# Kernel optimization log

Hardware: AMD Instinct MI355X
Metric: run time of the kernel (lower is better)

## Reference

```python
import jax, jax.numpy as jnp
import numpy as np

N_NODES = 10000
N_EDGES = 320000
IN_DIM = 128
HIDDEN = 256
NUM_LAYERS = 6
ALPHA = 0.1
LN_EPS = 1e-5


def setup_inputs() -> dict:
    key = jax.random.key(0)
    ks = jax.random.split(key, 12)
    x = jax.random.normal(ks[0], (N_NODES, IN_DIM), dtype=jnp.float32)
    edge_index = jax.random.randint(ks[1], (2, N_EDGES), 0, N_NODES, dtype=jnp.int64)
    # input MLP params
    W_in = jax.random.normal(ks[2], (IN_DIM, HIDDEN), dtype=jnp.float32) / np.sqrt(IN_DIM)
    b_in = jnp.zeros((HIDDEN,), dtype=jnp.float32)
    g_in = jnp.ones((HIDDEN,), dtype=jnp.float32)
    beta_in = jnp.zeros((HIDDEN,), dtype=jnp.float32)
    # per-layer GCNConv weight/bias + LayerNorm params, stacked over layers
    Wl = jax.random.normal(ks[3], (NUM_LAYERS, HIDDEN, HIDDEN), dtype=jnp.float32) / np.sqrt(HIDDEN)
    bl = jnp.zeros((NUM_LAYERS, HIDDEN), dtype=jnp.float32)
    gl = jnp.ones((NUM_LAYERS, HIDDEN), dtype=jnp.float32)
    betal = jnp.zeros((NUM_LAYERS, HIDDEN), dtype=jnp.float32)
    return {"x": x, "edge_index": edge_index, "W_in": W_in, "b_in": b_in,
            "g_in": g_in, "beta_in": beta_in, "Wl": Wl, "bl": bl,
            "gl": gl, "betal": betal}


def _layernorm(h, g, b):
    mu = jnp.mean(h, axis=-1, keepdims=True)
    var = jnp.var(h, axis=-1, keepdims=True)
    return (h - mu) * jax.lax.rsqrt(var + LN_EPS) * g + b


def reference(x, edge_index, W_in, b_in, g_in, beta_in, Wl, bl, gl, betal):
    N = x.shape[0]
    # input block: Linear -> GELU (exact erf) -> LayerNorm (dropout = eval identity)
    h = jax.nn.gelu(x @ W_in + b_in, approximate=False)
    h = _layernorm(h, g_in, beta_in)

    # GCN normalization with self loops, unit edge weights (edge_weight=None)
    loops = jnp.arange(N, dtype=edge_index.dtype)
    src = jnp.concatenate([edge_index[0], loops])  # [E+N] sources (j)
    dst = jnp.concatenate([edge_index[1], loops])  # [E+N] targets (i)
    w = jnp.ones((src.shape[0],), dtype=x.dtype)
    deg = jax.ops.segment_sum(w, dst, num_segments=N)
    dinv = jnp.where(deg > 0, deg ** -0.5, 0.0)
    norm = dinv[src] * w * dinv[dst]  # [E+N]

    h0 = h
    cur = h
    for l in range(NUM_LAYERS):
        m = cur @ Wl[l]                                        # [N,H] transform
        msgs = norm[:, None] * m[src]                          # gather + scale
        agg = jax.ops.segment_sum(msgs, dst, num_segments=N)   # scatter-add
        agg = agg + bl[l]
        hh = _layernorm(jax.nn.gelu(agg, approximate=False), gl[l], betal[l])
        cur = cur + (1.0 - ALPHA) * hh + ALPHA * h0
    return cur
```

## Files before the change

### kernel.cpp

```cpp
#include <hip/hip_runtime.h>
#include <math.h>

#define N_NODES   10000
#define N_EDGES   320000
#define IN_DIM    128
#define HIDDEN    256
#define NUM_LAYERS 6
#define ALPHA     0.1f
#define LN_EPS    1e-5f

__device__ __forceinline__ float gelu_exact(float x) {
    return 0.5f * x * (1.0f + erff(x * 0.70710678118654752440f));
}

__device__ __forceinline__ float wave_sum64(float v) {
#pragma unroll
    for (int i = 32; i > 0; i >>= 1) v += __shfl_xor(v, i);
    return v;
}


__global__ __launch_bounds__(256) void count_deg_kernel(const int* __restrict__ dst,
                                                        int* __restrict__ cnt) {
    int e = blockIdx.x * 256 + threadIdx.x;
    if (e < N_EDGES) atomicAdd(&cnt[dst[e]], 1);
}

__global__ __launch_bounds__(256) void dinv_kernel(const int* __restrict__ cnt,
                                                   float* __restrict__ dinv) {
    int i = blockIdx.x * 256 + threadIdx.x;
    if (i < N_NODES) dinv[i] = rsqrtf((float)(cnt[i] + 1));
}

__global__ __launch_bounds__(256) void scan_kernel(const int* __restrict__ cnt,
                                                   int* __restrict__ offs) {
    __shared__ int sums[256];
    __shared__ int bases[257];
    int t = threadIdx.x;
    const int chunk = (N_NODES + 255) / 256;
    int b0 = t * chunk;
    int b1 = b0 + chunk; if (b1 > N_NODES) b1 = N_NODES;
    if (b0 > N_NODES) b0 = N_NODES;
    int s = 0;
    for (int i = b0; i < b1; ++i) s += cnt[i];
    sums[t] = s;
    __syncthreads();
    if (t == 0) {
        int r = 0;
        for (int i = 0; i < 256; ++i) { bases[i] = r; r += sums[i]; }
        bases[256] = r;
    }
    __syncthreads();
    int r = bases[t];
    for (int i = b0; i < b1; ++i) { offs[i] = r; r += cnt[i]; }
    if (t == 0) offs[N_NODES] = bases[256];
}

__global__ __launch_bounds__(256) void fill_csr_kernel(const int* __restrict__ src,
                                                       const int* __restrict__ dst,
                                                       const int* __restrict__ offs,
                                                       int* __restrict__ cursor,
                                                       int* __restrict__ csr_src) {
    int e = blockIdx.x * 256 + threadIdx.x;
    if (e < N_EDGES) {
        int d = dst[e], s = src[e];
        int pos = atomicAdd(&cursor[d], 1);
        csr_src[offs[d] + pos] = s;
    }
}

template<int K>
__global__ __launch_bounds__(256) void gemm_kernel(const float* __restrict__ A,
                                                   const float* __restrict__ B,
                                                   float* __restrict__ C) {
    __shared__ float As[16][132];
    __shared__ float Bs[16][68];

    int tid = threadIdx.x;
    int tx = tid & 15;
    int ty = tid >> 4;
    int row0 = blockIdx.x * 128;
    int col0 = blockIdx.y * 64;

    float acc[8][4] = {};

    for (int k0 = 0; k0 < K; k0 += 16) {
        #pragma unroll
        for (int u = 0; u < 2; ++u) {
            int fi = tid * 2 + u;
            int r  = fi >> 2;
            int kk = (fi & 3) * 4;
            int row = row0 + r;
            if (row < N_NODES) {
                const float4 a4 = *(const float4*)&A[(size_t)row * K + k0 + kk];
                As[kk + 0][r] = a4.x; As[kk + 1][r] = a4.y;
                As[kk + 2][r] = a4.z; As[kk + 3][r] = a4.w;
            } else {
                As[kk + 0][r] = 0.f; As[kk + 1][r] = 0.f;
                As[kk + 2][r] = 0.f; As[kk + 3][r] = 0.f;
            }
        }
        {
            int rb = tid >> 4;
            int cb = (tid & 15) * 4;
            const float4 b4 = *(const float4*)&B[(size_t)(k0 + rb) * HIDDEN + col0 + cb];
            *(float4*)&Bs[rb][cb] = b4;
        }
        __syncthreads();

        #pragma unroll
        for (int kk = 0; kk < 16; ++kk) {
            const float4 al = *(const float4*)&As[kk][ty * 8 + 0];
            const float4 ah = *(const float4*)&As[kk][ty * 8 + 4];
            const float4 b4 = *(const float4*)&Bs[kk][tx * 4];
            float a[8] = {al.x, al.y, al.z, al.w, ah.x, ah.y, ah.z, ah.w};
            #pragma unroll
            for (int i = 0; i < 8; ++i) {
                acc[i][0] += a[i] * b4.x;
                acc[i][1] += a[i] * b4.y;
                acc[i][2] += a[i] * b4.z;
                acc[i][3] += a[i] * b4.w;
            }
        }
        __syncthreads();
    }

    #pragma unroll
    for (int i = 0; i < 8; ++i) {
        int row = row0 + ty * 8 + i;
        if (row < N_NODES) {
            float4 v = make_float4(acc[i][0], acc[i][1], acc[i][2], acc[i][3]);
            *(float4*)&C[(size_t)row * HIDDEN + col0 + tx * 4] = v;
        }
    }
}

__global__ __launch_bounds__(256) void ln_in_kernel(const float4* __restrict__ pre,
                                                    const float4* __restrict__ b4,
                                                    const float4* __restrict__ g4,
                                                    const float4* __restrict__ beta4,
                                                    float4* __restrict__ h0,
                                                    float4* __restrict__ cur) {
    int n = blockIdx.x * 4 + (threadIdx.x >> 6);
    int lane = threadIdx.x & 63;
    if (n >= N_NODES) return;

    float4 v = pre[(size_t)n * 64 + lane];
    float4 bb = b4[lane];
    float x0 = gelu_exact(v.x + bb.x);
    float x1 = gelu_exact(v.y + bb.y);
    float x2 = gelu_exact(v.z + bb.z);
    float x3 = gelu_exact(v.w + bb.w);

    float mu = wave_sum64(x0 + x1 + x2 + x3) * (1.0f / 256.0f);
    float d0 = x0 - mu, d1 = x1 - mu, d2 = x2 - mu, d3 = x3 - mu;
    float var = wave_sum64(d0 * d0 + d1 * d1 + d2 * d2 + d3 * d3) * (1.0f / 256.0f);
    float r = rsqrtf(var + LN_EPS);

    float4 gg = g4[lane], be = beta4[lane];
    float4 out = make_float4(d0 * r * gg.x + be.x, d1 * r * gg.y + be.y,
                             d2 * r * gg.z + be.z, d3 * r * gg.w + be.w);
    h0[(size_t)n * 64 + lane]  = out;
    cur[(size_t)n * 64 + lane] = out;
}

__global__ __launch_bounds__(256) void gather_q_kernel(const float4* __restrict__ m4,
                                                       const float* __restrict__ dinv,
                                                       const int* __restrict__ offs,
                                                       const int* __restrict__ csr_src,
                                                       const float4* __restrict__ bias4,
                                                       float4* __restrict__ pre4) {
    int i  = blockIdx.x;
    int q  = (i & 7) >> 1;
    int nb = (i >> 3) * 2 + (i & 1);
    int n  = nb * 4 + (threadIdx.x >> 6);
    int lane = threadIdx.x & 63;
    int g = lane >> 4;
    int t = lane & 15;
    int cbase = q * 16 + t;

    float dn = dinv[n];

    float4 acc = make_float4(0.f, 0.f, 0.f, 0.f);
    if (g == 0) {
        float4 sv = m4[(size_t)n * 64 + cbase];
        float dn2 = dn * dn;
        acc.x = sv.x * dn2; acc.y = sv.y * dn2; acc.z = sv.z * dn2; acc.w = sv.w * dn2;
    }

    int e1 = offs[n + 1];
    int ee = offs[n] + g;
    for (; ee + 12 < e1; ee += 16) {
        int sA = csr_src[ee];
        int sB = csr_src[ee + 4];
        int sC = csr_src[ee + 8];
        int sD = csr_src[ee + 12];
        float4 vA = m4[(size_t)sA * 64 + cbase];
        float4 vB = m4[(size_t)sB * 64 + cbase];
        float4 vC = m4[(size_t)sC * 64 + cbase];
        float4 vD = m4[(size_t)sD * 64 + cbase];
        float wA = dinv[sA] * dn;
        float wB = dinv[sB] * dn;
        float wC = dinv[sC] * dn;
        float wD = dinv[sD] * dn;
        acc.x += wA * vA.x + wB * vB.x + wC * vC.x + wD * vD.x;
        acc.y += wA * vA.y + wB * vB.y + wC * vC.y + wD * vD.y;
        acc.z += wA * vA.z + wB * vB.z + wC * vC.z + wD * vD.z;
        acc.w += wA * vA.w + wB * vB.w + wC * vC.w + wD * vD.w;
    }
    for (; ee < e1; ee += 4) {
        int s = csr_src[ee];
        float4 v = m4[(size_t)s * 64 + cbase];
        float w = dinv[s] * dn;
        acc.x += w * v.x; acc.y += w * v.y; acc.z += w * v.z; acc.w += w * v.w;
    }

    acc.x += __shfl_xor(acc.x, 16);
    acc.y += __shfl_xor(acc.y, 16);
    acc.z += __shfl_xor(acc.z, 16);
    acc.w += __shfl_xor(acc.w, 16);
    acc.x += __shfl_xor(acc.x, 32);
    acc.y += __shfl_xor(acc.y, 32);
    acc.z += __shfl_xor(acc.z, 32);
    acc.w += __shfl_xor(acc.w, 32);

    if (g == 0) {
        float4 bb = bias4[cbase];
        pre4[(size_t)n * 64 + cbase] = make_float4(acc.x + bb.x, acc.y + bb.y,
                                                   acc.z + bb.z, acc.w + bb.w);
    }
}

__global__ __launch_bounds__(256) void ln_res_kernel(const float4* __restrict__ pre4,
                                                     const float4* __restrict__ g4,
                                                     const float4* __restrict__ beta4,
                                                     const float4* __restrict__ h04,
                                                     float4* __restrict__ cur4) {
    int n = blockIdx.x * 4 + (threadIdx.x >> 6);
    int lane = threadIdx.x & 63;
    if (n >= N_NODES) return;

    float4 v = pre4[(size_t)n * 64 + lane];
    float x0 = gelu_exact(v.x);
    float x1 = gelu_exact(v.y);
    float x2 = gelu_exact(v.z);
    float x3 = gelu_exact(v.w);

    float mu = wave_sum64(x0 + x1 + x2 + x3) * (1.0f / 256.0f);
    float d0 = x0 - mu, d1 = x1 - mu, d2 = x2 - mu, d3 = x3 - mu;
    float var = wave_sum64(d0 * d0 + d1 * d1 + d2 * d2 + d3 * d3) * (1.0f / 256.0f);
    float r = rsqrtf(var + LN_EPS);

    float4 gg = g4[lane], be = beta4[lane];
    float h0v = d0 * r * gg.x + be.x;
    float h1v = d1 * r * gg.y + be.y;
    float h2v = d2 * r * gg.z + be.z;
    float h3v = d3 * r * gg.w + be.w;

    size_t idx = (size_t)n * 64 + lane;
    float4 c = cur4[idx];
    float4 h = h04[idx];
    float4 o = make_float4(c.x + (1.0f - ALPHA) * h0v + ALPHA * h.x,
                           c.y + (1.0f - ALPHA) * h1v + ALPHA * h.y,
                           c.z + (1.0f - ALPHA) * h2v + ALPHA * h.z,
                           c.w + (1.0f - ALPHA) * h3v + ALPHA * h.w);
    cur4[idx] = o;
}


extern "C" void kernel_launch(void* const* d_in, const int* in_sizes, int n_in,
                              void* d_out, int out_size, void* d_ws, size_t ws_size,
                              hipStream_t stream) {
    const float* x      = (const float*)d_in[0];
    const int*   ei     = (const int*)  d_in[1];
    const float* W_in   = (const float*)d_in[2];
    const float* b_in   = (const float*)d_in[3];
    const float* g_in   = (const float*)d_in[4];
    const float* bt_in  = (const float*)d_in[5];
    const float* Wl     = (const float*)d_in[6];
    const float* bl     = (const float*)d_in[7];
    const float* gl     = (const float*)d_in[8];
    const float* betal  = (const float*)d_in[9];

    const int* src = ei;
    const int* dst = ei + N_EDGES;

    float* cur = (float*)d_out;

    char* w = (char*)d_ws;
    size_t off = 0;
    auto alloc = [&](size_t bytes) -> void* {
        void* p = w + off;
        off = (off + bytes + 255) & ~(size_t)255;
        return p;
    };
    int*   cnt      = (int*)  alloc(N_NODES * sizeof(int));
    int*   cursor   = (int*)  alloc(N_NODES * sizeof(int));
    int*   offs     = (int*)  alloc((N_NODES + 1) * sizeof(int));
    float* dinv     = (float*)alloc(N_NODES * sizeof(float));
    int*   csr_src  = (int*)  alloc(N_EDGES * sizeof(int));
    float* h0       = (float*)alloc((size_t)N_NODES * HIDDEN * sizeof(float));
    float* m        = (float*)alloc((size_t)N_NODES * HIDDEN * sizeof(float));
    float* pre      = (float*)alloc((size_t)N_NODES * HIDDEN * sizeof(float));

    hipMemsetAsync(cnt,    0, N_NODES * sizeof(int), stream);
    hipMemsetAsync(cursor, 0, N_NODES * sizeof(int), stream);

    const int EB = (N_EDGES + 255) / 256;
    const int NB = (N_NODES + 255) / 256;
    const int NODE_BLOCKS = (N_NODES + 3) / 4;

    count_deg_kernel<<<EB, 256, 0, stream>>>(dst, cnt);
    dinv_kernel<<<NB, 256, 0, stream>>>(cnt, dinv);
    scan_kernel<<<1, 256, 0, stream>>>(cnt, offs);
    fill_csr_kernel<<<EB, 256, 0, stream>>>(src, dst, offs, cursor, csr_src);

    dim3 ggrid((N_NODES + 127) / 128, HIDDEN / 64);

    gemm_kernel<IN_DIM><<<ggrid, 256, 0, stream>>>(x, W_in, m);
    ln_in_kernel<<<NODE_BLOCKS, 256, 0, stream>>>((const float4*)m, (const float4*)b_in,
                                                  (const float4*)g_in, (const float4*)bt_in,
                                                  (float4*)h0, (float4*)cur);

    for (int l = 0; l < NUM_LAYERS; ++l) {
        gemm_kernel<HIDDEN><<<ggrid, 256, 0, stream>>>(cur, Wl + (size_t)l * HIDDEN * HIDDEN, m);
        gather_q_kernel<<<NODE_BLOCKS * 4, 256, 0, stream>>>((const float4*)m, dinv, offs, csr_src,
                                                             (const float4*)(bl + l * HIDDEN),
                                                             (float4*)pre);
        ln_res_kernel<<<NODE_BLOCKS, 256, 0, stream>>>((const float4*)pre,
                                                       (const float4*)(gl + l * HIDDEN),
                                                       (const float4*)(betal + l * HIDDEN),
                                                       (const float4*)h0, (float4*)cur);
    }
}
```

Measured before the change: 552.0 us.

## Replace FP32 SIMT GEMM with split-bf16 MFMA GEMM and pre-transposed weights

The scalar FP32 tiled GEMM is replaced by a matrix-core kernel. Each operand is split into bf16 hi and lo parts, and three MFMA 16x16x32 products (hi*hi, lo*hi, hi*lo) recover close to FP32 accuracy. A prep kernel transposes all layer weights and splits them into hi/lo bf16 arrays once per call, and activations are split on the fly while loading into shared memory. The aim is to cut GEMM compute time, at the cost of some precision loss and an extra prep launch.

```diff
diff --git a/kernel.cpp b/kernel.cpp
--- a/kernel.cpp
+++ b/kernel.cpp
@@ -9,6 +9,9 @@
 #define ALPHA     0.1f
 #define LN_EPS    1e-5f
 
+using bf16x8 = __attribute__((ext_vector_type(8))) __bf16;
+using f32x4  = __attribute__((ext_vector_type(4))) float;
+
 __device__ __forceinline__ float gelu_exact(float x) {
     return 0.5f * x * (1.0f + erff(x * 0.70710678118654752440f));
 }
@@ -17,6 +20,14 @@
 #pragma unroll
     for (int i = 32; i > 0; i >>= 1) v += __shfl_xor(v, i);
     return v;
+}
+
+__device__ __forceinline__ unsigned short f2bf(float f) {
+    unsigned u = __float_as_uint(f);
+    return (unsigned short)((u + 0x7FFF + ((u >> 16) & 1)) >> 16);
+}
+__device__ __forceinline__ float bf2f(unsigned short h) {
+    return __uint_as_float(((unsigned)h) << 16);
 }
 
 
@@ -69,70 +80,124 @@
     }
 }
 
+__global__ __launch_bounds__(256) void prep_w_kernel(const float* __restrict__ Wl,
+                                                     const float* __restrict__ W_in,
+                                                     unsigned short* __restrict__ hi,
+                                                     unsigned short* __restrict__ lo) {
+    int z = blockIdx.z;
+    const float* W;
+    unsigned short *ho, *lg;
+    int K;
+    if (z < 6) {
+        W = Wl + (size_t)z * HIDDEN * HIDDEN; K = HIDDEN;
+        ho = hi + (size_t)z * HIDDEN * HIDDEN;
+        lg = lo + (size_t)z * HIDDEN * HIDDEN;
+    } else {
+        W = W_in; K = IN_DIM;
+        ho = hi + (size_t)6 * HIDDEN * HIDDEN;
+        lg = lo + (size_t)6 * HIDDEN * HIDDEN;
+    }
+    int tk0 = blockIdx.x * 32;
+    if (tk0 >= K) return;
+    int tn0 = blockIdx.y * 32;
+
+    __shared__ float T[32][33];
+    int tx = threadIdx.x & 31, ty = threadIdx.x >> 5;
+    #pragma unroll
+    for (int i = 0; i < 32; i += 8)
+        T[ty + i][tx] = W[(size_t)(tk0 + ty + i) * HIDDEN + tn0 + tx];
+    __syncthreads();
+    #pragma unroll
+    for (int i = 0; i < 32; i += 8) {
+        int n = tn0 + ty + i, k = tk0 + tx;
+        float v = T[tx][ty + i];
+        unsigned short h = f2bf(v);
+        ho[(size_t)n * K + k] = h;
+        lg[(size_t)n * K + k] = f2bf(v - bf2f(h));
+    }
+}
+
 template<int K>
-__global__ __launch_bounds__(256) void gemm_kernel(const float* __restrict__ A,
-                                                   const float* __restrict__ B,
-                                                   float* __restrict__ C) {
-    __shared__ float As[16][132];
-    __shared__ float Bs[16][68];
-
-    int tid = threadIdx.x;
-    int tx = tid & 15;
-    int ty = tid >> 4;
-    int row0 = blockIdx.x * 128;
+__global__ __launch_bounds__(256) void gemm_mfma_kernel(const float* __restrict__ A,
+                                                        const unsigned short* __restrict__ Bh,
+                                                        const unsigned short* __restrict__ Bl,
+                                                        float* __restrict__ C) {
+    __shared__ unsigned short AsH[64][40];
+    __shared__ unsigned short AsL[64][40];
+    __shared__ unsigned short BsH[64][40];
+    __shared__ unsigned short BsL[64][40];
+
+    int tid  = threadIdx.x;
+    int row0 = blockIdx.x * 64;
     int col0 = blockIdx.y * 64;
 
-    float acc[8][4] = {};
-
-    for (int k0 = 0; k0 < K; k0 += 16) {
+    int l  = tid & 63, w = tid >> 6;
+    int wr = w >> 1, wc = w & 1;
+    int r  = l & 15, kb = l >> 4;
+
+    f32x4 acc00 = {0.f, 0.f, 0.f, 0.f};
+    f32x4 acc01 = acc00, acc10 = acc00, acc11 = acc00;
+
+    for (int k0 = 0; k0 < K; k0 += 32) {
+        __syncthreads();
         #pragma unroll
         for (int u = 0; u < 2; ++u) {
             int fi = tid * 2 + u;
-            int r  = fi >> 2;
-            int kk = (fi & 3) * 4;
-            int row = row0 + r;
-            if (row < N_NODES) {
-                const float4 a4 = *(const float4*)&A[(size_t)row * K + k0 + kk];
-                As[kk + 0][r] = a4.x; As[kk + 1][r] = a4.y;
-                As[kk + 2][r] = a4.z; As[kk + 3][r] = a4.w;
-            } else {
-                As[kk + 0][r] = 0.f; As[kk + 1][r] = 0.f;
-                As[kk + 2][r] = 0.f; As[kk + 3][r] = 0.f;
-            }
+            int row = fi >> 3, f4 = fi & 7;
+            float4 a = make_float4(0.f, 0.f, 0.f, 0.f);
+            if (row0 + row < N_NODES)
+                a = *(const float4*)&A[(size_t)(row0 + row) * K + k0 + f4 * 4];
+            unsigned short h0 = f2bf(a.x), h1 = f2bf(a.y), h2 = f2bf(a.z), h3 = f2bf(a.w);
+            *(short4*)&AsH[row][f4 * 4] = make_short4((short)h0, (short)h1, (short)h2, (short)h3);
+            *(short4*)&AsL[row][f4 * 4] = make_short4((short)f2bf(a.x - bf2f(h0)),
+                                                      (short)f2bf(a.y - bf2f(h1)),
+                                                      (short)f2bf(a.z - bf2f(h2)),
+                                                      (short)f2bf(a.w - bf2f(h3)));
         }
-        {
-            int rb = tid >> 4;
-            int cb = (tid & 15) * 4;
-            const float4 b4 = *(const float4*)&B[(size_t)(k0 + rb) * HIDDEN + col0 + cb];
-            *(float4*)&Bs[rb][cb] = b4;
+        #pragma unroll
+        for (int u = 0; u < 2; ++u) {
+            int fi = tid * 2 + u;
+            int row = fi >> 3, sg = fi & 7;
+            *(short4*)&BsH[row][sg * 4] = *(const short4*)&Bh[(size_t)(col0 + row) * K + k0 + sg * 4];
+            *(short4*)&BsL[row][sg * 4] = *(const short4*)&Bl[(size_t)(col0 + row) * K + k0 + sg * 4];
         }
         __syncthreads();
 
-        #pragma unroll
-        for (int kk = 0; kk < 16; ++kk) {
-            const float4 al = *(const float4*)&As[kk][ty * 8 + 0];
-            const float4 ah = *(const float4*)&As[kk][ty * 8 + 4];
-            const float4 b4 = *(const float4*)&Bs[kk][tx * 4];
-            float a[8] = {al.x, al.y, al.z, al.w, ah.x, ah.y, ah.z, ah.w};
-            #pragma unroll
-            for (int i = 0; i < 8; ++i) {
-                acc[i][0] += a[i] * b4.x;
-                acc[i][1] += a[i] * b4.y;
-                acc[i][2] += a[i] * b4.z;
-                acc[i][3] += a[i] * b4.w;
-            }
-        }
-        __syncthreads();
-    }
-
-    #pragma unroll
-    for (int i = 0; i < 8; ++i) {
-        int row = row0 + ty * 8 + i;
-        if (row < N_NODES) {
-            float4 v = make_float4(acc[i][0], acc[i][1], acc[i][2], acc[i][3]);
-            *(float4*)&C[(size_t)row * HIDDEN + col0 + tx * 4] = v;
-        }
-    }
+        bf16x8 ah0 = *(const bf16x8*)&AsH[wr * 32 +  0 + r][kb * 8];
+        bf16x8 ah1 = *(const bf16x8*)&AsH[wr * 32 + 16 + r][kb * 8];
+        bf16x8 al0 = *(const bf16x8*)&AsL[wr * 32 +  0 + r][kb * 8];
+        bf16x8 al1 = *(const bf16x8*)&AsL[wr * 32 + 16 + r][kb * 8];
+        bf16x8 bh0 = *(const bf16x8*)&BsH[wc * 32 +  0 + r][kb * 8];
+        bf16x8 bh1 = *(const bf16x8*)&BsH[wc * 32 + 16 + r][kb * 8];
+        bf16x8 bl0 = *(const bf16x8*)&BsL[wc * 32 +  0 + r][kb * 8];
+        bf16x8 bl1 = *(const bf16x8*)&BsL[wc * 32 + 16 + r][kb * 8];
+
+        acc00 = __builtin_amdgcn_mfma_f32_16x16x32_bf16(ah0, bh0, acc00, 0, 0, 0);
+        acc01 = __builtin_amdgcn_mfma_f32_16x16x32_bf16(ah0, bh1, acc01, 0, 0, 0);
+        acc10 = __builtin_amdgcn_mfma_f32_16x16x32_bf16(ah1, bh0, acc10, 0, 0, 0);
+        acc11 = __builtin_amdgcn_mfma_f32_16x16x32_bf16(ah1, bh1, acc11, 0, 0, 0);
+        acc00 = __builtin_amdgcn_mfma_f32_16x16x32_bf16(al0, bh0, acc00, 0, 0, 0);
+        acc01 = __builtin_amdgcn_mfma_f32_16x16x32_bf16(al0, bh1, acc01, 0, 0, 0);
+        acc10 = __builtin_amdgcn_mfma_f32_16x16x32_bf16(al1, bh0, acc10, 0, 0, 0);
+        acc11 = __builtin_amdgcn_mfma_f32_16x16x32_bf16(al1, bh1, acc11, 0, 0, 0);
+        acc00 = __builtin_amdgcn_mfma_f32_16x16x32_bf16(ah0, bl0, acc00, 0, 0, 0);
+        acc01 = __builtin_amdgcn_mfma_f32_16x16x32_bf16(ah0, bl1, acc01, 0, 0, 0);
+        acc10 = __builtin_amdgcn_mfma_f32_16x16x32_bf16(ah1, bl0, acc10, 0, 0, 0);
+        acc11 = __builtin_amdgcn_mfma_f32_16x16x32_bf16(ah1, bl1, acc11, 0, 0, 0);
+    }
+
+    #define WRITE_ACC(accv, i, j)                                              \
+    {                                                                          \
+        int gcol = col0 + wc * 32 + (j) * 16 + r;                              \
+        _Pragma("unroll")                                                      \
+        for (int reg = 0; reg < 4; ++reg) {                                    \
+            int grow = row0 + wr * 32 + (i) * 16 + kb * 4 + reg;               \
+            if (grow < N_NODES) C[(size_t)grow * HIDDEN + gcol] = accv[reg];   \
+        }                                                                      \
+    }
+    WRITE_ACC(acc00, 0, 0); WRITE_ACC(acc01, 0, 1);
+    WRITE_ACC(acc10, 1, 0); WRITE_ACC(acc11, 1, 1);
+    #undef WRITE_ACC
 }
 
 __global__ __launch_bounds__(256) void ln_in_kernel(const float4* __restrict__ pre,
@@ -294,6 +359,7 @@
         off = (off + bytes + 255) & ~(size_t)255;
         return p;
     };
+    const size_t WT_ELEMS = (size_t)6 * HIDDEN * HIDDEN + (size_t)HIDDEN * IN_DIM;
     int*   cnt      = (int*)  alloc(N_NODES * sizeof(int));
     int*   cursor   = (int*)  alloc(N_NODES * sizeof(int));
     int*   offs     = (int*)  alloc((N_NODES + 1) * sizeof(int));
@@ -302,6 +368,8 @@
     float* h0       = (float*)alloc((size_t)N_NODES * HIDDEN * sizeof(float));
     float* m        = (float*)alloc((size_t)N_NODES * HIDDEN * sizeof(float));
     float* pre      = (float*)alloc((size_t)N_NODES * HIDDEN * sizeof(float));
+    unsigned short* wt_hi = (unsigned short*)alloc(WT_ELEMS * sizeof(unsigned short));
+    unsigned short* wt_lo = (unsigned short*)alloc(WT_ELEMS * sizeof(unsigned short));
 
     hipMemsetAsync(cnt,    0, N_NODES * sizeof(int), stream);
     hipMemsetAsync(cursor, 0, N_NODES * sizeof(int), stream);
@@ -315,15 +383,21 @@
     scan_kernel<<<1, 256, 0, stream>>>(cnt, offs);
     fill_csr_kernel<<<EB, 256, 0, stream>>>(src, dst, offs, cursor, csr_src);
 
-    dim3 ggrid((N_NODES + 127) / 128, HIDDEN / 64);
-
-    gemm_kernel<IN_DIM><<<ggrid, 256, 0, stream>>>(x, W_in, m);
+    prep_w_kernel<<<dim3(8, 8, 7), 256, 0, stream>>>(Wl, W_in, wt_hi, wt_lo);
+
+    dim3 ggrid((N_NODES + 63) / 64, HIDDEN / 64);
+
+    const size_t IN_OFF = (size_t)6 * HIDDEN * HIDDEN;
+    gemm_mfma_kernel<IN_DIM><<<ggrid, 256, 0, stream>>>(x, wt_hi + IN_OFF, wt_lo + IN_OFF, m);
     ln_in_kernel<<<NODE_BLOCKS, 256, 0, stream>>>((const float4*)m, (const float4*)b_in,
                                                   (const float4*)g_in, (const float4*)bt_in,
                                                   (float4*)h0, (float4*)cur);
 
     for (int l = 0; l < NUM_LAYERS; ++l) {
-        gemm_kernel<HIDDEN><<<ggrid, 256, 0, stream>>>(cur, Wl + (size_t)l * HIDDEN * HIDDEN, m);
+        gemm_mfma_kernel<HIDDEN><<<ggrid, 256, 0, stream>>>(cur,
+                                                            wt_hi + (size_t)l * HIDDEN * HIDDEN,
+                                                            wt_lo + (size_t)l * HIDDEN * HIDDEN,
+                                                            m);
         gather_q_kernel<<<NODE_BLOCKS * 4, 256, 0, stream>>>((const float4*)m, dinv, offs, csr_src,
                                                              (const float4*)(bl + l * HIDDEN),
                                                              (float4*)pre);
```

Measured after the change: 451.5 us. 1.22x faster.
